# Optimization experiments

Measured on AMD Instinct MI355X. Metric: run time of the kernel, lower is better.

Reference implementation:

```python
import jax, jax.numpy as jnp
import numpy as np

# Static graph dimensions (mirror mat_wann config)
B, IN_DIM, NH, NO = 16384, 512, 128, 256
DENSITY = 0.03


def _build_adjacency():
    """Build the static sparse connectivity matrix.

    mat is [NH + NO, IN_DIM + NH]; entry values: 0 = no edge, 1 = linear edge
    (weight only), 2/3/4 = weight then tanh/relu/sigmoid. Hidden rows only read
    input columns (hidden->hidden block zero), output rows read inputs+hiddens.
    Edge order (for weight assignment) is row-major, as in the torch module.
    """
    rng = np.random.default_rng(0)
    p = DENSITY
    probs = [1.0 - p, p / 4, p / 4, p / 4, p / 4]
    mat_h = rng.choice(5, size=(NH, IN_DIM), p=probs)            # hidden rows (input cols only)
    mat_o = rng.choice(5, size=(NO, IN_DIM + NH), p=probs)       # output rows
    rows_h, cols_h = np.nonzero(mat_h)
    acts_h = mat_h[rows_h, cols_h]
    rows_o, cols_o = np.nonzero(mat_o)
    acts_o = mat_o[rows_o, cols_o]
    return (rows_h.astype(np.int32), cols_h.astype(np.int32), acts_h.astype(np.int32),
            rows_o.astype(np.int32), cols_o.astype(np.int32), acts_o.astype(np.int32))


def setup_inputs() -> dict:
    rows_h, cols_h, acts_h, rows_o, cols_o, acts_o = _build_adjacency()
    key = jax.random.key(0)
    kx, kh, ko = jax.random.split(key, 3)
    x = jax.random.normal(kx, (B, IN_DIM), dtype=jnp.float32)
    # one learned scalar weight per edge (nn.Linear(1,1,bias=False) each)
    wh = jax.random.normal(kh, (rows_h.shape[0],), dtype=jnp.float32) * 0.5
    wo = jax.random.normal(ko, (rows_o.shape[0],), dtype=jnp.float32) * 0.5
    return {
        "x": x, "wh": wh, "wo": wo,
        "rows_h": jnp.asarray(rows_h), "cols_h": jnp.asarray(cols_h), "acts_h": jnp.asarray(acts_h),
        "rows_o": jnp.asarray(rows_o), "cols_o": jnp.asarray(cols_o), "acts_o": jnp.asarray(acts_o),
    }


def _edge_act(z, acts):
    # act id 1 -> identity (weight only); 2 -> tanh; 3 -> relu; 4 -> sigmoid
    return jnp.where(acts == 2, jnp.tanh(z),
           jnp.where(acts == 3, jax.nn.relu(z),
           jnp.where(acts == 4, jax.nn.sigmoid(z), z)))


def reference(x, wh, wo, rows_h, cols_h, acts_h, rows_o, cols_o, acts_o):
    # hidden nodes: per-edge scalar weight + per-edge activation, scatter-add to dest
    zh = _edge_act(x[:, cols_h] * wh, acts_h)                     # [B, Eh]
    H = jnp.zeros((x.shape[0], NH), x.dtype).at[:, rows_h].add(zh)  # [B, NH]
    src = jnp.concatenate([x, H], axis=1)                         # [B, IN+NH]
    zo = _edge_act(src[:, cols_o] * wo, acts_o)                   # [B, Eo]
    out = jnp.zeros((x.shape[0], NO), x.dtype).at[:, rows_o].add(zo)
    return jnp.tanh(out)                                          # output_activation
```

## Files before the change

kernel.cpp:

```cpp
#include <hip/hip_runtime.h>
#include <math.h>

#define BATCH   16384
#define IN_DIM  512
#define NH      128
#define NO      256
#define L2E     1.4426950408889634f

__device__ __forceinline__ float fast_rcp(float x) { return __builtin_amdgcn_rcpf(x); }
__device__ __forceinline__ float fast_exp2(float x) {
#if __has_builtin(__builtin_amdgcn_exp2f)
    return __builtin_amdgcn_exp2f(x);
#else
    return exp2f(x);
#endif
}
__device__ __forceinline__ int rfl(int v) { return __builtin_amdgcn_readfirstlane(v); }

__device__ __forceinline__ float fast_tanh(float z) {
    float ex = fast_exp2(2.f * L2E * z);
    return 1.f - 2.f * fast_rcp(1.f + ex);
}
__device__ __forceinline__ float fast_sig(float z) {
    float ex = fast_exp2(-L2E * z);
    return fast_rcp(1.f + ex);
}
__device__ __forceinline__ float act_k(int a) {
    return (a == 2) ? (2.f * L2E) : ((a == 4) ? -L2E : 0.f);
}

__device__ __forceinline__ void acc_edge4(float4& acc, float4 v, float w, int a) {
    float zx = v.x * w, zy = v.y * w, zz = v.z * w, zw = v.w * w;
    if (a == 2) {
        acc.x += fast_tanh(zx); acc.y += fast_tanh(zy);
        acc.z += fast_tanh(zz); acc.w += fast_tanh(zw);
    } else if (a == 4) {
        acc.x += fast_sig(zx); acc.y += fast_sig(zy);
        acc.z += fast_sig(zz); acc.w += fast_sig(zw);
    } else if (a == 3) {
        acc.x += fmaxf(zx, 0.f); acc.y += fmaxf(zy, 0.f);
        acc.z += fmaxf(zz, 0.f); acc.w += fmaxf(zw, 0.f);
    } else {
        acc.x += zx; acc.y += zy; acc.z += zz; acc.w += zw;
    }
}

__device__ __forceinline__ unsigned int f2bf_rne(float f) {
    unsigned int u = __float_as_uint(f);
    return (u + 0x7FFFu + ((u >> 16) & 1u)) >> 16;
}
__device__ __forceinline__ float bf_lo(unsigned int u) { return __uint_as_float(u << 16); }
__device__ __forceinline__ float bf_hi(unsigned int u) { return __uint_as_float(u & 0xFFFF0000u); }

__device__ __forceinline__ int lower_bound_dev(const int* __restrict__ arr, int n, int v) {
    int lo = 0, hi = n;
    while (lo < hi) { int m = (lo + hi) >> 1; if (arr[m] < v) lo = m + 1; else hi = m; }
    return lo;
}

__device__ __forceinline__ void decode_bid(int bid, int rows_per_group, int& rb, int& rg) {
    int xcd = bid & 7;
    int k   = bid >> 3;
    int slice = xcd * 8 + (k & 7);
    rg = k >> 3;
    rb = slice * 256;
    (void)rows_per_group;
}

__global__ __launch_bounds__(256)
void prep_fused(const float* __restrict__ x, unsigned short* __restrict__ xt,
                const int* __restrict__ rows_h, const int* __restrict__ cols_h,
                const int* __restrict__ acts_h, const float* __restrict__ wh,
                const int* __restrict__ rows_o, const int* __restrict__ cols_o,
                const int* __restrict__ acts_o, const float* __restrict__ wo,
                int Eh, int Eo, int tile_blocks,
                int* __restrict__ offs_h, int* __restrict__ offs_o,
                int4* __restrict__ packed_h, int4* __restrict__ packed_o) {
    __shared__ float tile[64 * 65];
    if ((int)blockIdx.x < tile_blocks) {
        const int b0 = (blockIdx.x & (BATCH / 64 - 1)) * 64;
        const int c0 = (blockIdx.x / (BATCH / 64)) * 64;
        #pragma unroll
        for (int it = 0; it < 4; ++it) {
            int v = threadIdx.x + it * 256;
            int r = v >> 4, i = v & 15;
            const float4* row = (const float4*)(x + (size_t)(b0 + r) * IN_DIM + c0);
            float4 f = row[i];
            tile[r * 65 + i * 4 + 0] = f.x;
            tile[r * 65 + i * 4 + 1] = f.y;
            tile[r * 65 + i * 4 + 2] = f.z;
            tile[r * 65 + i * 4 + 3] = f.w;
        }
        __syncthreads();
        #pragma unroll
        for (int it = 0; it < 8; ++it) {
            int v = threadIdx.x + it * 256;
            int c = v >> 5, p = v & 31;
            int b = p * 2;
            unsigned int u = f2bf_rne(tile[b * 65 + c]) | (f2bf_rne(tile[(b + 1) * 65 + c]) << 16);
            *(unsigned int*)&xt[(size_t)(c0 + c) * BATCH + b0 + b] = u;
        }
        return;
    }
    int t = (blockIdx.x - tile_blocks) * 256 + threadIdx.x;
    if (t <= NH) offs_h[t] = lower_bound_dev(rows_h, Eh, t);
    else if (t <= NH + 1 + NO) offs_o[t - (NH + 1)] = lower_bound_dev(rows_o, Eo, t - (NH + 1));
    int u = t - (NH + 1 + NO + 1);
    if (u >= 0 && u < Eh) {
        int a = acts_h[u];
        packed_h[u] = make_int4(cols_h[u], a, __float_as_int(wh[u]), 0);
    }
    u -= Eh;
    if (u >= 0 && u < Eo) {
        int a = acts_o[u];
        packed_o[u] = make_int4(cols_o[u], a, __float_as_int(wo[u]), 0);
    }
}

__global__ __launch_bounds__(512)
void hidden_kernel(const unsigned short* __restrict__ xt, const int* __restrict__ offs_h,
                   const int4* __restrict__ packed_h, float* __restrict__ Ht) {
    const int lane = threadIdx.x & 63;
    const int wv   = threadIdx.x >> 6;
    int rb, rg;
    decode_bid(blockIdx.x, 8, rb, rg);
    const int bi = rb + lane * 4;
    const int r  = rg * 8 + wv;

    const int e0 = rfl(offs_h[r]);
    const int e1 = rfl(offs_h[r + 1]);
    float4 acc = make_float4(0.f, 0.f, 0.f, 0.f);
    #pragma unroll 4
    for (int e = e0; e < e1; ++e) {
        int4 p  = packed_h[e];
        int col = rfl(p.x);
        int a   = rfl(p.y);
        float w = __int_as_float(rfl(p.z));
        uint2 u = *(const uint2*)(xt + (size_t)col * BATCH + bi);
        float4 v = make_float4(bf_lo(u.x), bf_hi(u.x), bf_lo(u.y), bf_hi(u.y));
        acc_edge4(acc, v, w, a);
    }
    *(float4*)&Ht[(size_t)r * BATCH + bi] = acc;
}

#define OBS 260
__global__ __launch_bounds__(512)
void output_kernel(const unsigned short* __restrict__ xt, const float* __restrict__ Ht,
                   const int* __restrict__ offs_o, const int4* __restrict__ packed_o,
                   float* __restrict__ out) {
    __shared__ float OB[16 * OBS];
    const int lane = threadIdx.x & 63;
    const int wv   = threadIdx.x >> 6;
    int rb, rg;
    decode_bid(blockIdx.x, 16, rb, rg);
    const int r0 = rg * 16;
    const int bi = rb + lane * 4;

    #pragma unroll
    for (int rr = wv * 2; rr < wv * 2 + 2; ++rr) {
        const int r  = r0 + rr;
        const int e0 = rfl(offs_o[r]);
        const int e1 = rfl(offs_o[r + 1]);
        float4 acc = make_float4(0.f, 0.f, 0.f, 0.f);
        #pragma unroll 4
        for (int e = e0; e < e1; ++e) {
            int4 p  = packed_o[e];
            int col = rfl(p.x);
            int a   = rfl(p.y);
            float w = __int_as_float(rfl(p.z));
            float4 v;
            if (col < IN_DIM) {
                uint2 u = *(const uint2*)(xt + (size_t)col * BATCH + bi);
                v = make_float4(bf_lo(u.x), bf_hi(u.x), bf_lo(u.y), bf_hi(u.y));
            } else {
                v = *(const float4*)&Ht[(size_t)(col - IN_DIM) * BATCH + bi];
            }
            acc_edge4(acc, v, w, a);
        }
        OB[rr * OBS + lane * 4 + 0] = fast_tanh(acc.x);
        OB[rr * OBS + lane * 4 + 1] = fast_tanh(acc.y);
        OB[rr * OBS + lane * 4 + 2] = fast_tanh(acc.z);
        OB[rr * OBS + lane * 4 + 3] = fast_tanh(acc.w);
    }
    __syncthreads();
    #pragma unroll
    for (int it = 0; it < (256 * 16 / 4) / 512; ++it) {
        int v  = threadIdx.x + it * 512;
        int c4 = v & 3;
        int b  = v >> 2;
        float4 o;
        o.x = OB[(c4 * 4 + 0) * OBS + b];
        o.y = OB[(c4 * 4 + 1) * OBS + b];
        o.z = OB[(c4 * 4 + 2) * OBS + b];
        o.w = OB[(c4 * 4 + 3) * OBS + b];
        *(float4*)&out[(size_t)(rb + b) * NO + r0 + c4 * 4] = o;
    }
}

#define FT      1024
#define FBPB    64
#define FXS     514
#define FHS     65
#define FOBTS   260
#define FLDS    (99072 + 1544)
__device__ __forceinline__ unsigned short f2bf16s(float f) { return (unsigned short)f2bf_rne(f); }
__device__ __forceinline__ float bf2f(unsigned short h) { return __uint_as_float(((unsigned int)h) << 16); }
__device__ __forceinline__ float edge_act2(float z, int a, float k) {
    float ex = fast_exp2(k * z);
    float rc = fast_rcp(1.f + ex);
    return (a == 2) ? (1.f - 2.f * rc) : ((a == 4) ? rc : ((a == 3) ? fmaxf(z, 0.f) : z));
}
__global__ __launch_bounds__(FT)
void wann_fused(const float* __restrict__ x,
                const int* __restrict__ rows_h, const int* __restrict__ cols_h,
                const int* __restrict__ acts_h, const float* __restrict__ wh,
                const int* __restrict__ rows_o, const int* __restrict__ cols_o,
                const int* __restrict__ acts_o, const float* __restrict__ wo,
                float* __restrict__ out, int Eh, int Eo)
{
    extern __shared__ char lds[];
    unsigned short* X   = (unsigned short*)lds;
    float*          H   = (float*)(lds + 65792);
    float*          OBT = (float*)lds;
    int*            offsH = (int*)(lds + 99072);
    int*            offsO = offsH + (NH + 1);
    const int tid  = threadIdx.x;
    const int lane = tid & 63;
    const int wv   = tid >> 6;
    const int rb   = blockIdx.x * FBPB;
    const int* wh_i = (const int*)wh;
    const int* wo_i = (const int*)wo;
    {
        const float4* xv = (const float4*)(x + (size_t)rb * IN_DIM);
        #pragma unroll
        for (int kk = 0; kk < (FBPB * IN_DIM / 4) / FT; ++kk) {
            int v = tid + kk * FT;
            int r = v >> 7, i = v & 127;
            float4 f = xv[v];
            unsigned int lo = (unsigned int)f2bf16s(f.x) | ((unsigned int)f2bf16s(f.y) << 16);
            unsigned int hi = (unsigned int)f2bf16s(f.z) | ((unsigned int)f2bf16s(f.w) << 16);
            unsigned int* dst = (unsigned int*)&X[r * FXS + i * 4];
            dst[0] = lo; dst[1] = hi;
        }
    }
    if (tid <= NH) offsH[tid] = lower_bound_dev(rows_h, Eh, tid);
    else if (tid <= NH + 1 + NO) offsO[tid - (NH + 1)] = lower_bound_dev(rows_o, Eo, tid - (NH + 1));
    __syncthreads();
    for (int r = wv * (NH / 16); r < (wv + 1) * (NH / 16); ++r) {
        const int e0 = rfl(offsH[r]); const int e1 = rfl(offsH[r + 1]);
        float acc = 0.f;
        #pragma unroll 4
        for (int e = e0; e < e1; ++e) {
            int col = rfl(cols_h[e]); int a = rfl(acts_h[e]);
            float w = __int_as_float(rfl(wh_i[e]));
            acc += edge_act2(bf2f(X[lane * FXS + col]) * w, a, act_k(a));
        }
        H[r * FHS + lane] = acc;
    }
    __syncthreads();
    float res[NO / 16];
    #pragma unroll
    for (int rr = 0; rr < NO / 16; ++rr) {
        const int r = wv * (NO / 16) + rr;
        const int e0 = rfl(offsO[r]); const int e1 = rfl(offsO[r + 1]);
        float acc = 0.f;
        #pragma unroll 4
        for (int e = e0; e < e1; ++e) {
            int col = rfl(cols_o[e]); int a = rfl(acts_o[e]);
            float w = __int_as_float(rfl(wo_i[e]));
            float v = (col < IN_DIM) ? bf2f(X[lane * FXS + col]) : H[(col - IN_DIM) * FHS + lane];
            acc += edge_act2(v * w, a, act_k(a));
        }
        res[rr] = fast_tanh(acc);
    }
    __syncthreads();
    #pragma unroll
    for (int rr = 0; rr < NO / 16; ++rr)
        OBT[lane * FOBTS + wv * (NO / 16) + rr] = res[rr];
    __syncthreads();
    #pragma unroll
    for (int kk = 0; kk < (FBPB * NO / 4) / FT; ++kk) {
        int v = tid + kk * FT;
        int c4 = v & 63, b = v >> 6;
        float4 o = *(const float4*)&OBT[b * FOBTS + c4 * 4];
        *(float4*)&out[(size_t)(rb + b) * NO + c4 * 4] = o;
    }
}

extern "C" void kernel_launch(void* const* d_in, const int* in_sizes, int n_in,
                              void* d_out, int out_size, void* d_ws, size_t ws_size,
                              hipStream_t stream) {
    const float* x      = (const float*)d_in[0];
    const float* wh     = (const float*)d_in[1];
    const float* wo     = (const float*)d_in[2];
    const int*   rows_h = (const int*)d_in[3];
    const int*   cols_h = (const int*)d_in[4];
    const int*   acts_h = (const int*)d_in[5];
    const int*   rows_o = (const int*)d_in[6];
    const int*   cols_o = (const int*)d_in[7];
    const int*   acts_o = (const int*)d_in[8];
    float*       out    = (float*)d_out;

    const int Eh = in_sizes[1];
    const int Eo = in_sizes[2];

    char* ws = (char*)d_ws;
    int*  offs_h   = (int*)ws;
    int*  offs_o   = (int*)(ws + 1024);
    int4* packed_h = (int4*)(ws + 4096);
    int4* packed_o = packed_h + Eh;
    size_t tier_packed = 4096 + (size_t)(Eh + Eo) * 16;
    size_t xt_off      = (tier_packed + 255) & ~(size_t)255;
    unsigned short* xt = (unsigned short*)(ws + xt_off);
    size_t ht_off      = (xt_off + (size_t)IN_DIM * BATCH * 2 + 255) & ~(size_t)255;
    float* Ht          = (float*)(ws + ht_off);
    size_t need_full   = ht_off + (size_t)NH * BATCH * 4;

    const int ntasks      = (NH + 1) + (NO + 1) + Eh + Eo;
    const int edge_blocks = (ntasks + 255) / 256;
    const int tile_blocks = (BATCH / 64) * (IN_DIM / 64);

    if (ws_size >= need_full) {
        prep_fused<<<tile_blocks + edge_blocks, 256, 0, stream>>>(
            x, xt, rows_h, cols_h, acts_h, wh, rows_o, cols_o, acts_o, wo,
            Eh, Eo, tile_blocks, offs_h, offs_o, packed_h, packed_o);
        hidden_kernel<<<1024, 512, 0, stream>>>(xt, offs_h, packed_h, Ht);
        output_kernel<<<1024, 512, 0, stream>>>(xt, Ht, offs_o, packed_o, out);
    } else {
        wann_fused<<<BATCH / FBPB, FT, FLDS, stream>>>(
            x, rows_h, cols_h, acts_h, wh, rows_o, cols_o, acts_o, wo, out, Eh, Eo);
    }
}
```

Measured before the change: 140.9 us.

## Split output edges into input/hidden ranges and widen per-lane batch work

Prep now computes, for each output row, the edge index where input-column edges end and hidden-column edges begin. The output kernel runs two branch-free loops, one over bf16 x edges and one over fp32 H edges, instead of testing each column. Each lane now handles 8 batch elements with 16-byte loads, and blocks hold 1024 threads with one row per wave. The block-to-batch-slice mapping across XCDs is also reworked for both kernels. The wider per-lane work raises register pressure in exchange for fewer edge-metadata loads per element.

```diff
diff --git a/kernel.cpp b/kernel.cpp
--- a/kernel.cpp
+++ b/kernel.cpp
@@ -29,7 +29,22 @@
     return (a == 2) ? (2.f * L2E) : ((a == 4) ? -L2E : 0.f);
 }
 
-__device__ __forceinline__ void acc_edge4(float4& acc, float4 v, float w, int a) {
+__device__ __forceinline__ void acc_act8(float* acc, const float* v, float w, int a) {
+    if (a == 2) {
+        #pragma unroll
+        for (int j = 0; j < 8; ++j) acc[j] += fast_tanh(v[j] * w);
+    } else if (a == 4) {
+        #pragma unroll
+        for (int j = 0; j < 8; ++j) acc[j] += fast_sig(v[j] * w);
+    } else if (a == 3) {
+        #pragma unroll
+        for (int j = 0; j < 8; ++j) acc[j] += fmaxf(v[j] * w, 0.f);
+    } else {
+        #pragma unroll
+        for (int j = 0; j < 8; ++j) acc[j] += v[j] * w;
+    }
+}
+__device__ __forceinline__ void acc_act4(float4& acc, float4 v, float w, int a) {
     float zx = v.x * w, zy = v.y * w, zz = v.z * w, zw = v.w * w;
     if (a == 2) {
         acc.x += fast_tanh(zx); acc.y += fast_tanh(zy);
@@ -58,15 +73,6 @@
     return lo;
 }
 
-__device__ __forceinline__ void decode_bid(int bid, int rows_per_group, int& rb, int& rg) {
-    int xcd = bid & 7;
-    int k   = bid >> 3;
-    int slice = xcd * 8 + (k & 7);
-    rg = k >> 3;
-    rb = slice * 256;
-    (void)rows_per_group;
-}
-
 __global__ __launch_bounds__(256)
 void prep_fused(const float* __restrict__ x, unsigned short* __restrict__ xt,
                 const int* __restrict__ rows_h, const int* __restrict__ cols_h,
@@ -75,6 +81,7 @@
                 const int* __restrict__ acts_o, const float* __restrict__ wo,
                 int Eh, int Eo, int tile_blocks,
                 int* __restrict__ offs_h, int* __restrict__ offs_o,
+                int* __restrict__ split_o,
                 int4* __restrict__ packed_h, int4* __restrict__ packed_o) {
     __shared__ float tile[64 * 65];
     if ((int)blockIdx.x < tile_blocks) {
@@ -105,7 +112,18 @@
     int t = (blockIdx.x - tile_blocks) * 256 + threadIdx.x;
     if (t <= NH) offs_h[t] = lower_bound_dev(rows_h, Eh, t);
     else if (t <= NH + 1 + NO) offs_o[t - (NH + 1)] = lower_bound_dev(rows_o, Eo, t - (NH + 1));
-    int u = t - (NH + 1 + NO + 1);
+    int s = t - (NH + 1 + NO + 1);
+    if (s >= 0 && s < NO) {
+        int lo = 0, hi = Eo;
+        while (lo < hi) {
+            int m  = (lo + hi) >> 1;
+            int rm = rows_o[m];
+            bool less = (rm < s) || (rm == s && cols_o[m] < IN_DIM);
+            if (less) lo = m + 1; else hi = m;
+        }
+        split_o[s] = lo;
+    }
+    int u = t - (NH + 1 + NO + 1 + NO);
     if (u >= 0 && u < Eh) {
         int a = acts_h[u];
         packed_h[u] = make_int4(cols_h[u], a, __float_as_int(wh[u]), 0);
@@ -122,10 +140,14 @@
                    const int4* __restrict__ packed_h, float* __restrict__ Ht) {
     const int lane = threadIdx.x & 63;
     const int wv   = threadIdx.x >> 6;
-    int rb, rg;
-    decode_bid(blockIdx.x, 8, rb, rg);
-    const int bi = rb + lane * 4;
-    const int r  = rg * 8 + wv;
+    const int xcd  = blockIdx.x & 7;
+    const int m    = blockIdx.x >> 3;
+    const int rg   = m & 15;
+    const int u    = m >> 4;
+    const int s    = ((u >> 1) << 4) | (xcd << 1) | (u & 1);
+    const int rb   = s * 256;
+    const int bi   = rb + lane * 4;
+    const int r    = rg * 8 + wv;
 
     const int e0 = rfl(offs_h[r]);
     const int e1 = rfl(offs_h[r + 1]);
@@ -136,63 +158,83 @@
         int col = rfl(p.x);
         int a   = rfl(p.y);
         float w = __int_as_float(rfl(p.z));
-        uint2 u = *(const uint2*)(xt + (size_t)col * BATCH + bi);
-        float4 v = make_float4(bf_lo(u.x), bf_hi(u.x), bf_lo(u.y), bf_hi(u.y));
-        acc_edge4(acc, v, w, a);
+        uint2 uu = *(const uint2*)(xt + (size_t)col * BATCH + bi);
+        float4 v = make_float4(bf_lo(uu.x), bf_hi(uu.x), bf_lo(uu.y), bf_hi(uu.y));
+        acc_act4(acc, v, w, a);
     }
     *(float4*)&Ht[(size_t)r * BATCH + bi] = acc;
 }
 
-#define OBS 260
-__global__ __launch_bounds__(512)
+#define OBS2 516
+__global__ __launch_bounds__(1024)
 void output_kernel(const unsigned short* __restrict__ xt, const float* __restrict__ Ht,
-                   const int* __restrict__ offs_o, const int4* __restrict__ packed_o,
-                   float* __restrict__ out) {
-    __shared__ float OB[16 * OBS];
+                   const int* __restrict__ offs_o, const int* __restrict__ split_o,
+                   const int4* __restrict__ packed_o, float* __restrict__ out) {
+    __shared__ float OB[16 * OBS2];
     const int lane = threadIdx.x & 63;
     const int wv   = threadIdx.x >> 6;
-    int rb, rg;
-    decode_bid(blockIdx.x, 16, rb, rg);
-    const int r0 = rg * 16;
-    const int bi = rb + lane * 4;
+    const int xcd  = blockIdx.x & 7;
+    const int k    = blockIdx.x >> 3;
+    const int t    = ((k >> 4) << 3) | xcd;
+    const int rg   = k & 15;
+    const int rb   = t * 512;
+    const int r0   = rg * 16;
+    const int r    = r0 + wv;
+    const int bi   = rb + lane * 8;
+
+    const int e0 = rfl(offs_o[r]);
+    const int es = rfl(split_o[r]);
+    const int e1 = rfl(offs_o[r + 1]);
+
+    float acc[8] = {0.f, 0.f, 0.f, 0.f, 0.f, 0.f, 0.f, 0.f};
+    float v[8];
+
+    #pragma unroll 4
+    for (int e = e0; e < es; ++e) {
+        int4 p  = packed_o[e];
+        int col = rfl(p.x);
+        int a   = rfl(p.y);
+        float w = __int_as_float(rfl(p.z));
+        uint4 uu = *(const uint4*)(xt + (size_t)col * BATCH + bi);
+        v[0] = bf_lo(uu.x); v[1] = bf_hi(uu.x);
+        v[2] = bf_lo(uu.y); v[3] = bf_hi(uu.y);
+        v[4] = bf_lo(uu.z); v[5] = bf_hi(uu.z);
+        v[6] = bf_lo(uu.w); v[7] = bf_hi(uu.w);
+        acc_act8(acc, v, w, a);
+    }
+    #pragma unroll 4
+    for (int e = es; e < e1; ++e) {
+        int4 p  = packed_o[e];
+        int col = rfl(p.x) - IN_DIM;
+        int a   = rfl(p.y);
+        float w = __int_as_float(rfl(p.z));
+        const float* hp = Ht + (size_t)col * BATCH + bi;
+        float4 h0 = *(const float4*)hp;
+        float4 h1 = *(const float4*)(hp + 4);
+        v[0] = h0.x; v[1] = h0.y; v[2] = h0.z; v[3] = h0.w;
+        v[4] = h1.x; v[5] = h1.y; v[6] = h1.z; v[7] = h1.w;
+        acc_act8(acc, v, w, a);
+    }
+
+    float4 o0, o1;
+    o0.x = fast_tanh(acc[0]); o0.y = fast_tanh(acc[1]);
+    o0.z = fast_tanh(acc[2]); o0.w = fast_tanh(acc[3]);
+    o1.x = fast_tanh(acc[4]); o1.y = fast_tanh(acc[5]);
+    o1.z = fast_tanh(acc[6]); o1.w = fast_tanh(acc[7]);
+    *(float4*)&OB[wv * OBS2 + lane * 8 + 0] = o0;
+    *(float4*)&OB[wv * OBS2 + lane * 8 + 4] = o1;
+    __syncthreads();
 
     #pragma unroll
-    for (int rr = wv * 2; rr < wv * 2 + 2; ++rr) {
-        const int r  = r0 + rr;
-        const int e0 = rfl(offs_o[r]);
-        const int e1 = rfl(offs_o[r + 1]);
-        float4 acc = make_float4(0.f, 0.f, 0.f, 0.f);
-        #pragma unroll 4
-        for (int e = e0; e < e1; ++e) {
-            int4 p  = packed_o[e];
-            int col = rfl(p.x);
-            int a   = rfl(p.y);
-            float w = __int_as_float(rfl(p.z));
-            float4 v;
-            if (col < IN_DIM) {
-                uint2 u = *(const uint2*)(xt + (size_t)col * BATCH + bi);
-                v = make_float4(bf_lo(u.x), bf_hi(u.x), bf_lo(u.y), bf_hi(u.y));
-            } else {
-                v = *(const float4*)&Ht[(size_t)(col - IN_DIM) * BATCH + bi];
-            }
-            acc_edge4(acc, v, w, a);
-        }
-        OB[rr * OBS + lane * 4 + 0] = fast_tanh(acc.x);
-        OB[rr * OBS + lane * 4 + 1] = fast_tanh(acc.y);
-        OB[rr * OBS + lane * 4 + 2] = fast_tanh(acc.z);
-        OB[rr * OBS + lane * 4 + 3] = fast_tanh(acc.w);
-    }
-    __syncthreads();
-    #pragma unroll
-    for (int it = 0; it < (256 * 16 / 4) / 512; ++it) {
-        int v  = threadIdx.x + it * 512;
-        int c4 = v & 3;
-        int b  = v >> 2;
+    for (int it = 0; it < (512 * 16 / 4) / 1024; ++it) {
+        int vv = threadIdx.x + it * 1024;
+        int c4 = vv & 3;
+        int b  = vv >> 2;
         float4 o;
-        o.x = OB[(c4 * 4 + 0) * OBS + b];
-        o.y = OB[(c4 * 4 + 1) * OBS + b];
-        o.z = OB[(c4 * 4 + 2) * OBS + b];
-        o.w = OB[(c4 * 4 + 3) * OBS + b];
+        o.x = OB[(c4 * 4 + 0) * OBS2 + b];
+        o.y = OB[(c4 * 4 + 1) * OBS2 + b];
+        o.z = OB[(c4 * 4 + 2) * OBS2 + b];
+        o.w = OB[(c4 * 4 + 3) * OBS2 + b];
         *(float4*)&out[(size_t)(rb + b) * NO + r0 + c4 * 4] = o;
     }
 }
@@ -307,6 +349,7 @@
     char* ws = (char*)d_ws;
     int*  offs_h   = (int*)ws;
     int*  offs_o   = (int*)(ws + 1024);
+    int*  split_o  = (int*)(ws + 3072);
     int4* packed_h = (int4*)(ws + 4096);
     int4* packed_o = packed_h + Eh;
     size_t tier_packed = 4096 + (size_t)(Eh + Eo) * 16;
@@ -316,16 +359,16 @@
     float* Ht          = (float*)(ws + ht_off);
     size_t need_full   = ht_off + (size_t)NH * BATCH * 4;
 
-    const int ntasks      = (NH + 1) + (NO + 1) + Eh + Eo;
+    const int ntasks      = (NH + 1) + (NO + 1) + NO + Eh + Eo;
     const int edge_blocks = (ntasks + 255) / 256;
     const int tile_blocks = (BATCH / 64) * (IN_DIM / 64);
 
     if (ws_size >= need_full) {
         prep_fused<<<tile_blocks + edge_blocks, 256, 0, stream>>>(
             x, xt, rows_h, cols_h, acts_h, wh, rows_o, cols_o, acts_o, wo,
-            Eh, Eo, tile_blocks, offs_h, offs_o, packed_h, packed_o);
+            Eh, Eo, tile_blocks, offs_h, offs_o, split_o, packed_h, packed_o);
         hidden_kernel<<<1024, 512, 0, stream>>>(xt, offs_h, packed_h, Ht);
-        output_kernel<<<1024, 512, 0, stream>>>(xt, Ht, offs_o, packed_o, out);
+        output_kernel<<<512, 1024, 0, stream>>>(xt, Ht, offs_o, split_o, packed_o, out);
     } else {
         wann_fused<<<BATCH / FBPB, FT, FLDS, stream>>>(
             x, rows_h, cols_h, acts_h, wh, rows_o, cols_o, acts_o, wo, out, Eh, Eo);
```

Measured after the change: 141.0 us. About the same (+0.1%).

## Fuse prep, hidden and output stages into one cooperative kernel with grid syncs

Applied to the files above, without the earlier changes.

Replaces the three-kernel sequence (transpose/pack prep, hidden, output) with a single cooperative kernel of 1024 blocks of 512 threads that separates the stages with grid-wide syncs. This removes two kernel launches and their inter-kernel gaps. It also changes the block-to-batch-slice mapping so that different XCDs share slices differently, aiming at better L2 locality. Grid sync adds barrier cost and requires all 1024 blocks to be co-resident (launch bounds 512,8), and the code falls back to the old path if the cooperative launch fails.

```diff
diff --git a/kernel.cpp b/kernel.cpp
--- a/kernel.cpp
+++ b/kernel.cpp
@@ -1,5 +1,8 @@
 #include <hip/hip_runtime.h>
+#include <hip/hip_cooperative_groups.h>
 #include <math.h>
+
+namespace cg = cooperative_groups;
 
 #define BATCH   16384
 #define IN_DIM  512
@@ -29,7 +32,7 @@
     return (a == 2) ? (2.f * L2E) : ((a == 4) ? -L2E : 0.f);
 }
 
-__device__ __forceinline__ void acc_edge4(float4& acc, float4 v, float w, int a) {
+__device__ __forceinline__ void acc_act4(float4& acc, float4 v, float w, int a) {
     float zx = v.x * w, zy = v.y * w, zz = v.z * w, zw = v.w * w;
     if (a == 2) {
         acc.x += fast_tanh(zx); acc.y += fast_tanh(zy);
@@ -58,13 +61,158 @@
     return lo;
 }
 
-__device__ __forceinline__ void decode_bid(int bid, int rows_per_group, int& rb, int& rg) {
+__device__ __forceinline__ float4 run_hidden_row(const unsigned short* __restrict__ xt,
+                                                 const int4* __restrict__ packed_h,
+                                                 int e0, int e1, int bi) {
+    float4 acc = make_float4(0.f, 0.f, 0.f, 0.f);
+    #pragma unroll 4
+    for (int e = e0; e < e1; ++e) {
+        int4 p  = packed_h[e];
+        int col = rfl(p.x);
+        int a   = rfl(p.y);
+        float w = __int_as_float(rfl(p.z));
+        uint2 uu = *(const uint2*)(xt + (size_t)col * BATCH + bi);
+        float4 v = make_float4(bf_lo(uu.x), bf_hi(uu.x), bf_lo(uu.y), bf_hi(uu.y));
+        acc_act4(acc, v, w, a);
+    }
+    return acc;
+}
+__device__ __forceinline__ float4 run_output_row(const unsigned short* __restrict__ xt,
+                                                 const float* __restrict__ Ht,
+                                                 const int4* __restrict__ packed_o,
+                                                 int e0, int e1, int bi) {
+    float4 acc = make_float4(0.f, 0.f, 0.f, 0.f);
+    #pragma unroll 4
+    for (int e = e0; e < e1; ++e) {
+        int4 p  = packed_o[e];
+        int col = rfl(p.x);
+        int a   = rfl(p.y);
+        float w = __int_as_float(rfl(p.z));
+        float4 v;
+        if (col < IN_DIM) {
+            uint2 uu = *(const uint2*)(xt + (size_t)col * BATCH + bi);
+            v = make_float4(bf_lo(uu.x), bf_hi(uu.x), bf_lo(uu.y), bf_hi(uu.y));
+        } else {
+            v = *(const float4*)&Ht[(size_t)(col - IN_DIM) * BATCH + bi];
+        }
+        acc_act4(acc, v, w, a);
+    }
+    return acc;
+}
+
+__device__ __forceinline__ void decode_slice(int bid, int& s, int& rg) {
     int xcd = bid & 7;
-    int k   = bid >> 3;
-    int slice = xcd * 8 + (k & 7);
-    rg = k >> 3;
-    rb = slice * 256;
-    (void)rows_per_group;
+    int m   = bid >> 3;
+    rg      = m & 15;
+    int u   = m >> 4;
+    s = ((u >> 1) << 4) | (xcd << 1) | (u & 1);
+}
+
+#define OBS 260
+__global__ __launch_bounds__(512, 8)
+void wann_coop(const float* __restrict__ x,
+               const int* __restrict__ rows_h, const int* __restrict__ cols_h,
+               const int* __restrict__ acts_h, const float* __restrict__ wh,
+               const int* __restrict__ rows_o, const int* __restrict__ cols_o,
+               const int* __restrict__ acts_o, const float* __restrict__ wo,
+               float* __restrict__ out, int Eh, int Eo,
+               unsigned short* __restrict__ xt, float* __restrict__ Ht,
+               int* __restrict__ offs_h, int* __restrict__ offs_o,
+               int4* __restrict__ packed_h, int4* __restrict__ packed_o)
+{
+    __shared__ float smem[64 * 129];
+    cg::grid_group grid = cg::this_grid();
+    const int tid  = threadIdx.x;
+    const int lane = tid & 63;
+    const int wv   = tid >> 6;
+    const int bid  = blockIdx.x;
+
+    {
+        const int bt = bid >> 2, ct = bid & 3;
+        const int b0 = bt * 64, c0 = ct * 128;
+        #pragma unroll
+        for (int it = 0; it < 4; ++it) {
+            int r = (tid >> 5) + it * 16;
+            int i = tid & 31;
+            float4 f = *(const float4*)&x[(size_t)(b0 + r) * IN_DIM + c0 + i * 4];
+            float* d = &smem[r * 129 + i * 4];
+            d[0] = f.x; d[1] = f.y; d[2] = f.z; d[3] = f.w;
+        }
+        __syncthreads();
+        {
+            int col  = tid >> 2;
+            int part = tid & 3;
+            unsigned int u[8];
+            #pragma unroll
+            for (int j = 0; j < 8; ++j) {
+                float lo = smem[(part * 16 + 2 * j)     * 129 + col];
+                float hi = smem[(part * 16 + 2 * j + 1) * 129 + col];
+                u[j] = f2bf_rne(lo) | (f2bf_rne(hi) << 16);
+            }
+            size_t base = (size_t)(c0 + col) * BATCH + b0 + part * 16;
+            *(uint4*)&xt[base]     = make_uint4(u[0], u[1], u[2], u[3]);
+            *(uint4*)&xt[base + 8] = make_uint4(u[4], u[5], u[6], u[7]);
+        }
+        int g = bid * 512 + tid;
+        if (g <= NH) offs_h[g] = lower_bound_dev(rows_h, Eh, g);
+        else if (g <= NH + 1 + NO) offs_o[g - (NH + 1)] = lower_bound_dev(rows_o, Eo, g - (NH + 1));
+        int u2 = g - (NH + 1 + NO + 1);
+        if (u2 >= 0 && u2 < Eh) {
+            int a = acts_h[u2];
+            packed_h[u2] = make_int4(cols_h[u2], a, __float_as_int(wh[u2]), 0);
+        }
+        u2 -= Eh;
+        if (u2 >= 0 && u2 < Eo) {
+            int a = acts_o[u2];
+            packed_o[u2] = make_int4(cols_o[u2], a, __float_as_int(wo[u2]), 0);
+        }
+    }
+    grid.sync();
+
+    {
+        int s, rg;
+        decode_slice(bid, s, rg);
+        const int bi = s * 256 + lane * 4;
+        const int r  = rg * 8 + wv;
+        const int e0 = rfl(offs_h[r]);
+        const int e1 = rfl(offs_h[r + 1]);
+        float4 acc = run_hidden_row(xt, packed_h, e0, e1, bi);
+        *(float4*)&Ht[(size_t)r * BATCH + bi] = acc;
+    }
+    grid.sync();
+
+    {
+        float* OB = smem;
+        int s, rg;
+        decode_slice(bid, s, rg);
+        const int rb = s * 256;
+        const int r0 = rg * 16;
+        const int bi = rb + lane * 4;
+        #pragma unroll
+        for (int rr = wv * 2; rr < wv * 2 + 2; ++rr) {
+            const int r  = r0 + rr;
+            const int e0 = rfl(offs_o[r]);
+            const int e1 = rfl(offs_o[r + 1]);
+            float4 acc = run_output_row(xt, Ht, packed_o, e0, e1, bi);
+            OB[rr * OBS + lane * 4 + 0] = fast_tanh(acc.x);
+            OB[rr * OBS + lane * 4 + 1] = fast_tanh(acc.y);
+            OB[rr * OBS + lane * 4 + 2] = fast_tanh(acc.z);
+            OB[rr * OBS + lane * 4 + 3] = fast_tanh(acc.w);
+        }
+        __syncthreads();
+        #pragma unroll
+        for (int it = 0; it < 2; ++it) {
+            int v  = tid + it * 512;
+            int c4 = v & 3;
+            int b  = v >> 2;
+            float4 o;
+            o.x = OB[(c4 * 4 + 0) * OBS + b];
+            o.y = OB[(c4 * 4 + 1) * OBS + b];
+            o.z = OB[(c4 * 4 + 2) * OBS + b];
+            o.w = OB[(c4 * 4 + 3) * OBS + b];
+            *(float4*)&out[(size_t)(rb + b) * NO + r0 + c4 * 4] = o;
+        }
+    }
 }
 
 __global__ __launch_bounds__(256)
@@ -122,28 +270,16 @@
                    const int4* __restrict__ packed_h, float* __restrict__ Ht) {
     const int lane = threadIdx.x & 63;
     const int wv   = threadIdx.x >> 6;
-    int rb, rg;
-    decode_bid(blockIdx.x, 8, rb, rg);
-    const int bi = rb + lane * 4;
+    int s, rg;
+    decode_slice(blockIdx.x, s, rg);
+    const int bi = s * 256 + lane * 4;
     const int r  = rg * 8 + wv;
-
     const int e0 = rfl(offs_h[r]);
     const int e1 = rfl(offs_h[r + 1]);
-    float4 acc = make_float4(0.f, 0.f, 0.f, 0.f);
-    #pragma unroll 4
-    for (int e = e0; e < e1; ++e) {
-        int4 p  = packed_h[e];
-        int col = rfl(p.x);
-        int a   = rfl(p.y);
-        float w = __int_as_float(rfl(p.z));
-        uint2 u = *(const uint2*)(xt + (size_t)col * BATCH + bi);
-        float4 v = make_float4(bf_lo(u.x), bf_hi(u.x), bf_lo(u.y), bf_hi(u.y));
-        acc_edge4(acc, v, w, a);
-    }
+    float4 acc = run_hidden_row(xt, packed_h, e0, e1, bi);
     *(float4*)&Ht[(size_t)r * BATCH + bi] = acc;
 }
 
-#define OBS 260
 __global__ __launch_bounds__(512)
 void output_kernel(const unsigned short* __restrict__ xt, const float* __restrict__ Ht,
                    const int* __restrict__ offs_o, const int4* __restrict__ packed_o,
@@ -151,32 +287,17 @@
     __shared__ float OB[16 * OBS];
     const int lane = threadIdx.x & 63;
     const int wv   = threadIdx.x >> 6;
-    int rb, rg;
-    decode_bid(blockIdx.x, 16, rb, rg);
+    int s, rg;
+    decode_slice(blockIdx.x, s, rg);
+    const int rb = s * 256;
     const int r0 = rg * 16;
     const int bi = rb + lane * 4;
-
     #pragma unroll
     for (int rr = wv * 2; rr < wv * 2 + 2; ++rr) {
         const int r  = r0 + rr;
         const int e0 = rfl(offs_o[r]);
         const int e1 = rfl(offs_o[r + 1]);
-        float4 acc = make_float4(0.f, 0.f, 0.f, 0.f);
-        #pragma unroll 4
-        for (int e = e0; e < e1; ++e) {
-            int4 p  = packed_o[e];
-            int col = rfl(p.x);
-            int a   = rfl(p.y);
-            float w = __int_as_float(rfl(p.z));
-            float4 v;
-            if (col < IN_DIM) {
-                uint2 u = *(const uint2*)(xt + (size_t)col * BATCH + bi);
-                v = make_float4(bf_lo(u.x), bf_hi(u.x), bf_lo(u.y), bf_hi(u.y));
-            } else {
-                v = *(const float4*)&Ht[(size_t)(col - IN_DIM) * BATCH + bi];
-            }
-            acc_edge4(acc, v, w, a);
-        }
+        float4 acc = run_output_row(xt, Ht, packed_o, e0, e1, bi);
         OB[rr * OBS + lane * 4 + 0] = fast_tanh(acc.x);
         OB[rr * OBS + lane * 4 + 1] = fast_tanh(acc.y);
         OB[rr * OBS + lane * 4 + 2] = fast_tanh(acc.z);
@@ -184,7 +305,7 @@
     }
     __syncthreads();
     #pragma unroll
-    for (int it = 0; it < (256 * 16 / 4) / 512; ++it) {
+    for (int it = 0; it < 2; ++it) {
         int v  = threadIdx.x + it * 512;
         int c4 = v & 3;
         int b  = v >> 2;
@@ -301,8 +422,8 @@
     const int*   acts_o = (const int*)d_in[8];
     float*       out    = (float*)d_out;
 
-    const int Eh = in_sizes[1];
-    const int Eo = in_sizes[2];
+    int Eh = in_sizes[1];
+    int Eo = in_sizes[2];
 
     char* ws = (char*)d_ws;
     int*  offs_h   = (int*)ws;
@@ -316,16 +437,27 @@
     float* Ht          = (float*)(ws + ht_off);
     size_t need_full   = ht_off + (size_t)NH * BATCH * 4;
 
-    const int ntasks      = (NH + 1) + (NO + 1) + Eh + Eo;
-    const int edge_blocks = (ntasks + 255) / 256;
-    const int tile_blocks = (BATCH / 64) * (IN_DIM / 64);
-
     if (ws_size >= need_full) {
-        prep_fused<<<tile_blocks + edge_blocks, 256, 0, stream>>>(
-            x, xt, rows_h, cols_h, acts_h, wh, rows_o, cols_o, acts_o, wo,
-            Eh, Eo, tile_blocks, offs_h, offs_o, packed_h, packed_o);
-        hidden_kernel<<<1024, 512, 0, stream>>>(xt, offs_h, packed_h, Ht);
-        output_kernel<<<1024, 512, 0, stream>>>(xt, Ht, offs_o, packed_o, out);
+        void* kargs[] = {
+            (void*)&x, (void*)&rows_h, (void*)&cols_h, (void*)&acts_h, (void*)&wh,
+            (void*)&rows_o, (void*)&cols_o, (void*)&acts_o, (void*)&wo,
+            (void*)&out, (void*)&Eh, (void*)&Eo,
+            (void*)&xt, (void*)&Ht, (void*)&offs_h, (void*)&offs_o,
+            (void*)&packed_h, (void*)&packed_o };
+        hipError_t err = hipLaunchCooperativeKernel((const void*)wann_coop,
+                                                    dim3(1024), dim3(512),
+                                                    kargs, 0, stream);
+        if (err != hipSuccess) {
+            (void)hipGetLastError();
+            const int ntasks      = (NH + 1) + (NO + 1) + Eh + Eo;
+            const int edge_blocks = (ntasks + 255) / 256;
+            const int tile_blocks = (BATCH / 64) * (IN_DIM / 64);
+            prep_fused<<<tile_blocks + edge_blocks, 256, 0, stream>>>(
+                x, xt, rows_h, cols_h, acts_h, wh, rows_o, cols_o, acts_o, wo,
+                Eh, Eo, tile_blocks, offs_h, offs_o, packed_h, packed_o);
+            hidden_kernel<<<1024, 512, 0, stream>>>(xt, offs_h, packed_h, Ht);
+            output_kernel<<<1024, 512, 0, stream>>>(xt, Ht, offs_o, packed_o, out);
+        }
     } else {
         wann_fused<<<BATCH / FBPB, FT, FLDS, stream>>>(
             x, rows_h, cols_h, acts_h, wh, rows_o, cols_o, acts_o, wo, out, Eh, Eo);
```

Result: slower. 392.9 us (+178.9%).
